# Performance work log

Hardware: AMD Instinct MI355X
Metric: run time of the kernel (lower is better)

Reference implementation:

```python
import jax, jax.numpy as jnp
import numpy as np

SEQ, BATCH, IN, HID = 2048, 4096, 4, 3


def setup_inputs() -> dict:
    key = jax.random.key(0)
    ks = jax.random.split(key, 6)
    s = 1.0 / np.sqrt(HID)  # PyTorch RNN init scale
    return {
        "x": jax.random.normal(ks[0], (SEQ, BATCH, IN), dtype=jnp.float32),
        "h0": jax.random.normal(ks[1], (1, BATCH, HID), dtype=jnp.float32),
        "W_ih": jax.random.uniform(ks[2], (HID, IN), minval=-s, maxval=s, dtype=jnp.float32),
        "W_hh": jax.random.uniform(ks[3], (HID, HID), minval=-s, maxval=s, dtype=jnp.float32),
        "b_ih": jax.random.uniform(ks[4], (HID,), minval=-s, maxval=s, dtype=jnp.float32),
        "b_hh": jax.random.uniform(ks[5], (HID,), minval=-s, maxval=s, dtype=jnp.float32),
    }


def reference(x, h0, W_ih, W_hh, b_ih, b_hh):
    # Single-layer ReLU RNN (batch_first=False):
    #   h_t = relu(x_t @ W_ih^T + b_ih + h_{t-1} @ W_hh^T + b_hh)
    # Precompute the input projection for all timesteps (vectorized GEMM),
    # then scan only the tiny recurrent update.
    pre = jnp.einsum('tbi,hi->tbh', x, W_ih) + b_ih + b_hh  # [T,B,H]

    def step(h, pre_t):
        h_new = jax.nn.relu(pre_t + h @ W_hh.T)  # [B,H]
        return h_new, h_new

    h_last, outs = jax.lax.scan(step, h0[0], pre)
    return outs, h_last[None]  # ([T,B,H], [1,B,H]) as nn.RNN returns
```

## Files before the change

kernel.cpp:

```cpp
#include <hip/hip_runtime.h>

#define T_SEQ  2048
#define BATCH  4096
#define CHUNK  16
#define NCHUNK (T_SEQ / CHUNK)
#define XR     6
#define PR     2
#define NS     6
#define LOOK   4
#define NITER  (NCHUNK + 2)

typedef float v4f __attribute__((ext_vector_type(4)));
struct Out3 { float a, b, c; };

#define AS1c(p) ((const __attribute__((address_space(1))) void*)(p))
#define AS3(p)  ((__attribute__((address_space(3))) void*)(p))

#define BARRIER() do {                              \
    __builtin_amdgcn_sched_barrier(0);              \
    asm volatile("s_barrier" ::: "memory");         \
    __builtin_amdgcn_sched_barrier(0);              \
} while (0)

__global__ __launch_bounds__(512, 1) void rnn_fused(
    const float* __restrict__ x,
    const float* __restrict__ h0,
    const float* __restrict__ Wih,
    const float* __restrict__ Whh,
    const float* __restrict__ bih,
    const float* __restrict__ bhh,
    float* __restrict__ out)
{
    __shared__ v4f xs[XR * CHUNK * 64];
    __shared__ v4f ps[PR * CHUNK * 64];

    const int tid  = threadIdx.x;
    const int lane = tid & 63;
    const int wid  = tid >> 6;
    const int b    = blockIdx.x * 64 + lane;

    const v4f* __restrict__ xg = (const v4f*)x;

#define STAGE(c) do {                                                          \
        const int _s0 = ((c) % XR) * CHUNK;                                    \
        _Pragma("unroll")                                                      \
        for (int _u = 0; _u < CHUNK; ++_u) {                                   \
            __builtin_amdgcn_global_load_lds(                                  \
                AS1c(xg + (size_t)((c) * CHUNK + _u) * BATCH + b),             \
                AS3(&xs[(_s0 + _u) * 64]), 16, 0, 0);                          \
        }                                                                      \
    } while (0)

    if (wid >= 2) {
        const int s = wid - 2;
        if (s < LOOK) STAGE(s);
        int nstage = (s < LOOK) ? (s + NS) : s;
        int nwait  = s;
#pragma unroll 1
        for (int i = 0; i < NITER; ++i) {
            if (nstage < NCHUNK && i + LOOK == nstage) { STAGE(nstage); nstage += NS; }
            if (i == nwait) {
                asm volatile("s_waitcnt vmcnt(0)" ::: "memory");
                nwait += NS;
            }
            BARRIER();
        }
    } else if (wid == 1) {
        const float w00 = Wih[0], w01 = Wih[1], w02 = Wih[2],  w03 = Wih[3];
        const float w10 = Wih[4], w11 = Wih[5], w12 = Wih[6],  w13 = Wih[7];
        const float w20 = Wih[8], w21 = Wih[9], w22 = Wih[10], w23 = Wih[11];
        const float bb0 = bih[0] + bhh[0];
        const float bb1 = bih[1] + bhh[1];
        const float bb2 = bih[2] + bhh[2];
#pragma unroll 1
        for (int i = 0; i < NITER; ++i) {
            const int cp = i - 1;
            if (cp >= 0 && cp < NCHUNK) {
                const v4f* __restrict__ xr = &xs[((cp % XR) * CHUNK) * 64 + lane];
                v4f* __restrict__ pw = &ps[((cp & (PR - 1)) * CHUNK) * 64 + lane];
#pragma unroll
                for (int u = 0; u < CHUNK; ++u) {
                    v4f xv = xr[u * 64];
                    float p0 = fmaf(w00, xv.x, fmaf(w01, xv.y,
                               fmaf(w02, xv.z, fmaf(w03, xv.w, bb0))));
                    float p1 = fmaf(w10, xv.x, fmaf(w11, xv.y,
                               fmaf(w12, xv.z, fmaf(w13, xv.w, bb1))));
                    float p2 = fmaf(w20, xv.x, fmaf(w21, xv.y,
                               fmaf(w22, xv.z, fmaf(w23, xv.w, bb2))));
                    v4f pv; pv.x = p0; pv.y = p1; pv.z = p2; pv.w = 0.0f;
                    pw[u * 64] = pv;
                }
                asm volatile("s_waitcnt lgkmcnt(0)" ::: "memory");
            }
            BARRIER();
        }
    } else {
        const float a00 = Whh[0], a01 = Whh[1], a02 = Whh[2];
        const float a10 = Whh[3], a11 = Whh[4], a12 = Whh[5];
        const float a20 = Whh[6], a21 = Whh[7], a22 = Whh[8];
        float h0r = h0[b * 3 + 0];
        float h1r = h0[b * 3 + 1];
        float h2r = h0[b * 3 + 2];
        Out3* __restrict__ ob = (Out3*)out;
#pragma unroll 1
        for (int i = 0; i < NITER; ++i) {
            const int cc = i - 2;
            if (cc >= 0) {
                const v4f* __restrict__ pr = &ps[((cc & (PR - 1)) * CHUNK) * 64 + lane];
                Out3* __restrict__ obase = ob + (size_t)cc * CHUNK * BATCH + b;
#pragma unroll
                for (int u = 0; u < CHUNK; ++u) {
                    v4f pv = pr[u * 64];
                    float t0 = fmaf(a00, h0r, fmaf(a01, h1r, fmaf(a02, h2r, pv.x)));
                    float t1 = fmaf(a10, h0r, fmaf(a11, h1r, fmaf(a12, h2r, pv.y)));
                    float t2 = fmaf(a20, h0r, fmaf(a21, h1r, fmaf(a22, h2r, pv.z)));
                    h0r = fmaxf(t0, 0.0f);
                    h1r = fmaxf(t1, 0.0f);
                    h2r = fmaxf(t2, 0.0f);
                    obase[(size_t)u * BATCH] = Out3{h0r, h1r, h2r};
                }
            }
            BARRIER();
        }
        Out3* lastp = (Out3*)(out + (size_t)T_SEQ * BATCH * 3);
        lastp[b] = Out3{h0r, h1r, h2r};
    }
#undef STAGE
}

extern "C" void kernel_launch(void* const* d_in, const int* in_sizes, int n_in,
                              void* d_out, int out_size, void* d_ws, size_t ws_size,
                              hipStream_t stream) {
    const float* x   = (const float*)d_in[0];
    const float* h0  = (const float*)d_in[1];
    const float* Wih = (const float*)d_in[2];
    const float* Whh = (const float*)d_in[3];
    const float* bih = (const float*)d_in[4];
    const float* bhh = (const float*)d_in[5];
    float* out = (float*)d_out;

    rnn_fused<<<BATCH / 64, 512, 0, stream>>>(x, h0, Wih, Whh, bih, bhh, out);
}
```

Measured before the change: 263.8 us.

## Split hidden units across quad lanes with DPP broadcast, 16 batches per block

Each batch element's recurrence is now handled by four lanes, one per hidden unit (three active), with DPP quad broadcasts exchanging hidden state. This shortens the serial dependency chain per timestep and raises the block count from 64 to 256, so more CUs are used. The separate input-projection wave and its LDS buffer are removed, and the projection is fused into the recurrence wave. Staging now uses 64-timestep chunks across three loader waves. The trade-off is that a quarter of the recurrence lanes sit idle, output stores become scalar per lane, and each block carries less batch parallelism.

```diff
diff --git a/kernel.cpp b/kernel.cpp
--- a/kernel.cpp
+++ b/kernel.cpp
@@ -1,17 +1,16 @@
 #include <hip/hip_runtime.h>
 
-#define T_SEQ  2048
-#define BATCH  4096
-#define CHUNK  16
-#define NCHUNK (T_SEQ / CHUNK)
-#define XR     6
-#define PR     2
-#define NS     6
-#define LOOK   4
-#define NITER  (NCHUNK + 2)
+#define T_SEQ   2048
+#define BATCH   4096
+#define BPB     16
+#define NBLK    (BATCH / BPB)
+#define CHUNK   64
+#define NCHUNK  (T_SEQ / CHUNK)
+#define XR      4
+#define NS      3
+#define NITER   (NCHUNK + 1)
 
 typedef float v4f __attribute__((ext_vector_type(4)));
-struct Out3 { float a, b, c; };
 
 #define AS1c(p) ((const __attribute__((address_space(1))) void*)(p))
 #define AS3(p)  ((__attribute__((address_space(3))) void*)(p))
@@ -22,7 +21,11 @@
     __builtin_amdgcn_sched_barrier(0);              \
 } while (0)
 
-__global__ __launch_bounds__(512, 1) void rnn_fused(
+#define QBCAST(hf, pat) \
+    __builtin_bit_cast(float, __builtin_amdgcn_mov_dpp( \
+        __builtin_bit_cast(int, (hf)), (pat), 0xF, 0xF, true))
+
+__global__ __launch_bounds__(256, 1) void rnn_fused(
     const float* __restrict__ x,
     const float* __restrict__ h0,
     const float* __restrict__ Wih,
@@ -31,101 +34,77 @@
     const float* __restrict__ bhh,
     float* __restrict__ out)
 {
-    __shared__ v4f xs[XR * CHUNK * 64];
-    __shared__ v4f ps[PR * CHUNK * 64];
+    __shared__ v4f xs[XR * CHUNK * BPB];
 
     const int tid  = threadIdx.x;
     const int lane = tid & 63;
     const int wid  = tid >> 6;
-    const int b    = blockIdx.x * 64 + lane;
+    const int b0   = blockIdx.x * BPB;
 
-    const v4f* __restrict__ xg = (const v4f*)x;
+    if (wid > 0) {
+        const int s = wid - 1;
+        const v4f* __restrict__ xg = (const v4f*)x;
+        const int vlo = (lane >> 4) * BATCH + b0 + (lane & 15);
 
 #define STAGE(c) do {                                                          \
-        const int _s0 = ((c) % XR) * CHUNK;                                    \
+        const int _slot = ((c) & (XR - 1)) * (CHUNK * BPB);                    \
         _Pragma("unroll")                                                      \
-        for (int _u = 0; _u < CHUNK; ++_u) {                                   \
+        for (int _g = 0; _g < CHUNK / 4; ++_g) {                               \
             __builtin_amdgcn_global_load_lds(                                  \
-                AS1c(xg + (size_t)((c) * CHUNK + _u) * BATCH + b),             \
-                AS3(&xs[(_s0 + _u) * 64]), 16, 0, 0);                          \
+                AS1c(xg + ((size_t)(c) * CHUNK + _g * 4) * BATCH + vlo),       \
+                AS3(&xs[_slot + _g * (4 * BPB)]), 16, 0, 0);                   \
         }                                                                      \
     } while (0)
 
-    if (wid >= 2) {
-        const int s = wid - 2;
-        if (s < LOOK) STAGE(s);
-        int nstage = (s < LOOK) ? (s + NS) : s;
-        int nwait  = s;
+        if (s == 0) STAGE(0);
+        if (s == 1) STAGE(1);
 #pragma unroll 1
         for (int i = 0; i < NITER; ++i) {
-            if (nstage < NCHUNK && i + LOOK == nstage) { STAGE(nstage); nstage += NS; }
-            if (i == nwait) {
+            const int ci = i + 2;
+            if (ci < NCHUNK && (ci % NS) == s) STAGE(ci);
+            if (i < NCHUNK && (i % NS) == s)
                 asm volatile("s_waitcnt vmcnt(0)" ::: "memory");
-                nwait += NS;
-            }
             BARRIER();
         }
-    } else if (wid == 1) {
-        const float w00 = Wih[0], w01 = Wih[1], w02 = Wih[2],  w03 = Wih[3];
-        const float w10 = Wih[4], w11 = Wih[5], w12 = Wih[6],  w13 = Wih[7];
-        const float w20 = Wih[8], w21 = Wih[9], w22 = Wih[10], w23 = Wih[11];
-        const float bb0 = bih[0] + bhh[0];
-        const float bb1 = bih[1] + bhh[1];
-        const float bb2 = bih[2] + bhh[2];
+#undef STAGE
+    } else {
+        const int bi = lane >> 2;
+        const int j  = lane & 3;
+        const int jj = (j < 3) ? j : 2;
+
+        const float w0 = Wih[jj * 4 + 0], w1 = Wih[jj * 4 + 1];
+        const float w2 = Wih[jj * 4 + 2], w3 = Wih[jj * 4 + 3];
+        const float a0 = Whh[jj * 3 + 0], a1 = Whh[jj * 3 + 1];
+        const float a2 = Whh[jj * 3 + 2];
+        const float bb = bih[jj] + bhh[jj];
+
+        float h = h0[(b0 + bi) * 3 + jj];
+        const size_t ooff = (size_t)(b0 + bi) * 3 + j;
+
 #pragma unroll 1
         for (int i = 0; i < NITER; ++i) {
-            const int cp = i - 1;
-            if (cp >= 0 && cp < NCHUNK) {
-                const v4f* __restrict__ xr = &xs[((cp % XR) * CHUNK) * 64 + lane];
-                v4f* __restrict__ pw = &ps[((cp & (PR - 1)) * CHUNK) * 64 + lane];
+            const int c = i - 1;
+            if (c >= 0 && j < 3) {
+                const v4f* __restrict__ xr = &xs[(c & (XR - 1)) * (CHUNK * BPB) + bi];
+                float* __restrict__ op = out + (size_t)c * CHUNK * (BATCH * 3) + ooff;
 #pragma unroll
-                for (int u = 0; u < CHUNK; ++u) {
-                    v4f xv = xr[u * 64];
-                    float p0 = fmaf(w00, xv.x, fmaf(w01, xv.y,
-                               fmaf(w02, xv.z, fmaf(w03, xv.w, bb0))));
-                    float p1 = fmaf(w10, xv.x, fmaf(w11, xv.y,
-                               fmaf(w12, xv.z, fmaf(w13, xv.w, bb1))));
-                    float p2 = fmaf(w20, xv.x, fmaf(w21, xv.y,
-                               fmaf(w22, xv.z, fmaf(w23, xv.w, bb2))));
-                    v4f pv; pv.x = p0; pv.y = p1; pv.z = p2; pv.w = 0.0f;
-                    pw[u * 64] = pv;
-                }
-                asm volatile("s_waitcnt lgkmcnt(0)" ::: "memory");
-            }
-            BARRIER();
-        }
-    } else {
-        const float a00 = Whh[0], a01 = Whh[1], a02 = Whh[2];
-        const float a10 = Whh[3], a11 = Whh[4], a12 = Whh[5];
-        const float a20 = Whh[6], a21 = Whh[7], a22 = Whh[8];
-        float h0r = h0[b * 3 + 0];
-        float h1r = h0[b * 3 + 1];
-        float h2r = h0[b * 3 + 2];
-        Out3* __restrict__ ob = (Out3*)out;
-#pragma unroll 1
-        for (int i = 0; i < NITER; ++i) {
-            const int cc = i - 2;
-            if (cc >= 0) {
-                const v4f* __restrict__ pr = &ps[((cc & (PR - 1)) * CHUNK) * 64 + lane];
-                Out3* __restrict__ obase = ob + (size_t)cc * CHUNK * BATCH + b;
-#pragma unroll
-                for (int u = 0; u < CHUNK; ++u) {
-                    v4f pv = pr[u * 64];
-                    float t0 = fmaf(a00, h0r, fmaf(a01, h1r, fmaf(a02, h2r, pv.x)));
-                    float t1 = fmaf(a10, h0r, fmaf(a11, h1r, fmaf(a12, h2r, pv.y)));
-                    float t2 = fmaf(a20, h0r, fmaf(a21, h1r, fmaf(a22, h2r, pv.z)));
-                    h0r = fmaxf(t0, 0.0f);
-                    h1r = fmaxf(t1, 0.0f);
-                    h2r = fmaxf(t2, 0.0f);
-                    obase[(size_t)u * BATCH] = Out3{h0r, h1r, h2r};
+                for (int tt = 0; tt < CHUNK; ++tt) {
+                    v4f xv = xr[tt * BPB];
+                    float p = fmaf(w0, xv.x, fmaf(w1, xv.y,
+                              fmaf(w2, xv.z, fmaf(w3, xv.w, bb))));
+                    float g0 = QBCAST(h, 0x00);
+                    float g1 = QBCAST(h, 0x55);
+                    float g2 = QBCAST(h, 0xAA);
+                    float t0 = fmaf(a0, g0, fmaf(a1, g1, fmaf(a2, g2, p)));
+                    h = fmaxf(t0, 0.0f);
+                    op[(size_t)tt * (BATCH * 3)] = h;
                 }
             }
             BARRIER();
         }
-        Out3* lastp = (Out3*)(out + (size_t)T_SEQ * BATCH * 3);
-        lastp[b] = Out3{h0r, h1r, h2r};
+        if (j < 3)
+            out[(size_t)T_SEQ * BATCH * 3 + ooff] = h;
     }
-#undef STAGE
 }
 
 extern "C" void kernel_launch(void* const* d_in, const int* in_sizes, int n_in,
@@ -139,5 +118,5 @@
     const float* bhh = (const float*)d_in[5];
     float* out = (float*)d_out;
 
-    rnn_fused<<<BATCH / 64, 512, 0, stream>>>(x, h0, Wih, Whh, bih, bhh, out);
+    rnn_fused<<<NBLK, 256, 0, stream>>>(x, h0, Wih, Whh, bih, bhh, out);
 }
```

Result: faster. 250.7 us (-4.9%).
